# Kernel optimization log

Hardware: AMD Instinct MI355X
Metric: run time of the kernel (lower is better)

## Reference

```python
import jax, jax.numpy as jnp
import numpy as np

N = 50000      # nodes
E = 800000     # edges (avg degree 16)
D = 128        # node_embedding_dim
H = 256        # hidden_dim


def setup_inputs() -> dict:
    key = jax.random.key(0)
    ks = jax.random.split(key, 12)
    init = lambda k, shape, fan: (jax.random.normal(k, shape, jnp.float32) / np.sqrt(fan).astype(np.float32))
    return {
        "node_ids": jnp.arange(N, dtype=jnp.int32),
        "edge_index": jax.random.randint(ks[0], (2, E), 0, N, jnp.int32),
        "neighbour_edge_index": jax.random.randint(ks[1], (2, E), 0, N, jnp.int32),
        "edge_attr": jax.random.uniform(ks[2], (E,), jnp.float32),
        "emb": init(ks[3], (N, D), D),          # Embedding table
        "W_in": init(ks[4], (D, H), D), "b_in": jnp.zeros((H,), jnp.float32),
        "W_out": init(ks[5], (H, D), H), "b_out": jnp.zeros((D,), jnp.float32),
        "W1": init(ks[6], (2 * D, D), 2 * D), "b1": jnp.zeros((D,), jnp.float32),
        "W2": init(ks[7], (D, D), D), "b2": jnp.zeros((D,), jnp.float32),
        "W3": init(ks[8], (D, 1), D), "b3": jnp.zeros((1,), jnp.float32),
    }


def gcn_conv(x, W, b, edge_index, w):
    """PyG GCNConv, add_self_loops=False, normalize=True.
    out_i = b + sum_{(j->i)} d_i^{-1/2} w_ji d_j^{-1/2} (x_j @ W)
    deg_i = sum of incoming edge weights at target node i.
    """
    row, col = edge_index[0], edge_index[1]
    deg = jax.ops.segment_sum(w, col, num_segments=N)
    dinv = jnp.where(deg > 0, 1.0 / jnp.sqrt(deg), 0.0)
    norm = dinv[row] * w * dinv[col]                    # [E]
    h = x @ W                                           # [N, out]
    msg = h[row] * norm[:, None]                        # [E, out]
    return jax.ops.segment_sum(msg, col, num_segments=N) + b


def reference(node_ids, edge_index, neighbour_edge_index, edge_attr,
              emb, W_in, b_in, W_out, b_out, W1, b1, W2, b2, W3, b3):
    x = emb[node_ids]                                   # embedding lookup [N, D]
    x = jax.nn.elu(gcn_conv(x, W_in, b_in, edge_index, edge_attr))
    ones = jnp.ones((neighbour_edge_index.shape[1],), x.dtype)
    x = jax.nn.elu(gcn_conv(x, W_out, b_out, neighbour_edge_index, ones))
    # edge-level gather-concat-MLP decoder
    src, dst = edge_index[0], edge_index[1]
    h = jnp.concatenate([x[src], x[dst]], axis=1)       # [E, 2D]
    h = jax.nn.relu(h @ W1 + b1)
    h = jax.nn.relu(h @ W2 + b2)
    return (h @ W3 + b3).squeeze(-1)                    # [E]
```

## Files before the change

kernel.cpp:

```cpp
#include <hip/hip_runtime.h>
#include <math.h>

#define NN 50000
#define NE 800000

typedef __attribute__((ext_vector_type(8))) short s8_t;
typedef __attribute__((ext_vector_type(4))) float f4_t;

__device__ __forceinline__ short bf16_rne(float v) {
  unsigned u = __float_as_uint(v);
  unsigned r = (u + 0x7FFFu + ((u >> 16) & 1u)) >> 16;
  return (short)r;
}
__device__ __forceinline__ float bf16_tof(short h) {
  return __uint_as_float(((unsigned)(unsigned short)h) << 16);
}
__device__ __forceinline__ void split2(float v, short& hi, short& lo) {
  hi = bf16_rne(v);
  lo = bf16_rne(v - bf16_tof(hi));
}


__global__ __launch_bounds__(256) void k_wcvt(const float* __restrict__ W1,
                                              const float* __restrict__ W2,
                                              const float* __restrict__ W_in,
                                              const float* __restrict__ W_out,
                                              short* __restrict__ w1th,
                                              short* __restrict__ w1tl,
                                              short* __restrict__ w2th,
                                              short* __restrict__ w2tl,
                                              short* __restrict__ winth,
                                              short* __restrict__ wintl,
                                              short* __restrict__ woutth,
                                              short* __restrict__ wouttl) {
  int i = blockIdx.x * 256 + threadIdx.x;
  if (i < 32768) {
    int k = i >> 7, n = i & 127;
    short h, l; split2(W1[i], h, l);
    w1th[n * 256 + k] = h; w1tl[n * 256 + k] = l;
  } else if (i < 49152) {
    int j = i - 32768;
    int k = j >> 7, n = j & 127;
    short h, l; split2(W2[j], h, l);
    w2th[n * 128 + k] = h; w2tl[n * 128 + k] = l;
  } else if (i < 81920) {
    int j = i - 49152;
    int k = j >> 8, n = j & 255;
    short h, l; split2(W_in[j], h, l);
    winth[n * 128 + k] = h; wintl[n * 128 + k] = l;
  } else if (i < 114688) {
    int j = i - 81920;
    int k = j >> 7, n = j & 127;
    short h, l; split2(W_out[j], h, l);
    woutth[n * 256 + k] = h; wouttl[n * 256 + k] = l;
  }
}


__global__ __launch_bounds__(256) void k_hist(const int* __restrict__ ei,
                                              const int* __restrict__ nei,
                                              const float* __restrict__ w,
                                              int* __restrict__ cnt1,
                                              float* __restrict__ deg1,
                                              int* __restrict__ cnt2) {
  int e = blockIdx.x * 256 + threadIdx.x;
  if (e < NE) {
    int c1 = ei[NE + e];
    atomicAdd(&cnt1[c1], 1);
    atomicAdd(&deg1[c1], w[e]);
    atomicAdd(&cnt2[nei[NE + e]], 1);
  }
}

__global__ __launch_bounds__(256) void k_dinvs(const float* __restrict__ deg1,
                                               const int* __restrict__ cnt2,
                                               float* __restrict__ dinv1,
                                               float* __restrict__ dinv2) {
  int i = blockIdx.x * 256 + threadIdx.x;
  if (i < NN) {
    float d1 = deg1[i];
    dinv1[i] = d1 > 0.f ? (1.0f / sqrtf(d1)) : 0.f;
    int c2 = cnt2[i];
    dinv2[i] = c2 > 0 ? (1.0f / sqrtf((float)c2)) : 0.f;
  }
}


#define NCHUNK 196

__global__ __launch_bounds__(256) void k_scan_part(const int* __restrict__ cnt1,
                                                   const int* __restrict__ cnt2,
                                                   int* __restrict__ part) {
  int g = blockIdx.x >= NCHUNK;
  int chunk = g ? blockIdx.x - NCHUNK : blockIdx.x;
  const int* cnt = g ? cnt2 : cnt1;
  int i = chunk * 256 + threadIdx.x;
  int v = (i < NN) ? cnt[i] : 0;
  __shared__ int sd[4];
#pragma unroll
  for (int o = 32; o; o >>= 1) v += __shfl_down(v, o);
  if ((threadIdx.x & 63) == 0) sd[threadIdx.x >> 6] = v;
  __syncthreads();
  if (threadIdx.x == 0) part[blockIdx.x] = sd[0] + sd[1] + sd[2] + sd[3];
}

__global__ __launch_bounds__(256) void k_scan_mid(int* __restrict__ part,
                                                  int* __restrict__ off1_last,
                                                  int* __restrict__ off2_last) {
  __shared__ int sd[256];
  for (int g = 0; g < 2; g++) {
    int base = g * NCHUNK;
    int v = (threadIdx.x < NCHUNK) ? part[base + threadIdx.x] : 0;
    sd[threadIdx.x] = v;
    __syncthreads();
    for (int o = 1; o < 256; o <<= 1) {
      int x = (threadIdx.x >= o) ? sd[threadIdx.x - o] : 0;
      __syncthreads();
      sd[threadIdx.x] += x;
      __syncthreads();
    }
    if (threadIdx.x < NCHUNK) part[base + threadIdx.x] = sd[threadIdx.x] - v;
    if (threadIdx.x == 255) *(g ? off2_last : off1_last) = sd[255];
    __syncthreads();
  }
}

__global__ __launch_bounds__(256) void k_scan_final(const int* __restrict__ cnt1,
                                                    const int* __restrict__ cnt2,
                                                    const int* __restrict__ part,
                                                    int* __restrict__ off1,
                                                    int* __restrict__ pos1,
                                                    int* __restrict__ off2,
                                                    int* __restrict__ pos2) {
  int g = blockIdx.x >= NCHUNK;
  int chunk = g ? blockIdx.x - NCHUNK : blockIdx.x;
  const int* cnt = g ? cnt2 : cnt1;
  int* off = g ? off2 : off1;
  int* pos = g ? pos2 : pos1;
  __shared__ int sd[256];
  int i = chunk * 256 + threadIdx.x;
  int v = (i < NN) ? cnt[i] : 0;
  sd[threadIdx.x] = v;
  __syncthreads();
  for (int o = 1; o < 256; o <<= 1) {
    int x = (threadIdx.x >= o) ? sd[threadIdx.x - o] : 0;
    __syncthreads();
    sd[threadIdx.x] += x;
    __syncthreads();
  }
  if (i < NN) {
    int ex = part[blockIdx.x] + sd[threadIdx.x] - v;
    off[i] = ex; pos[i] = ex;
  }
}


__global__ __launch_bounds__(256) void k_fill(const int* __restrict__ ei,
                                              const int* __restrict__ nei,
                                              const float* __restrict__ w,
                                              const float* __restrict__ dinv1,
                                              const float* __restrict__ dinv2,
                                              int* __restrict__ pos1,
                                              int4* __restrict__ c1pack,
                                              int* __restrict__ pos2,
                                              int2* __restrict__ c2pack) {
  int e = blockIdx.x * 256 + threadIdx.x;
  if (e < NE) {
    int r = ei[e], c = ei[NE + e];
    float nv = dinv1[r] * w[e] * dinv1[c];
    int s = atomicAdd(&pos1[c], 1);
    c1pack[s] = make_int4(r, c, e, __float_as_int(nv));
    int r2 = nei[e], c2v = nei[NE + e];
    float nv2 = dinv2[r2] * dinv2[c2v];
    int s2 = atomicAdd(&pos2[c2v], 1);
    c2pack[s2] = make_int2(r2, __float_as_int(nv2));
  }
}


__global__ __launch_bounds__(256) void k_agg1(const int* __restrict__ off,
                                              const int4* __restrict__ c1pack,
                                              const int* __restrict__ ids,
                                              const float* __restrict__ emb,
                                              short* __restrict__ aggXh,
                                              short* __restrict__ aggXl) {
  int wave = threadIdx.x >> 6, lane = threadIdx.x & 63;
  int h = lane >> 5, sub = lane & 31;
  int node = blockIdx.x * 4 + wave;
  int start = off[node], end = off[node + 1];
  float4 acc = make_float4(0.f, 0.f, 0.f, 0.f);
  int i = start + h;
  for (; i + 14 < end; i += 16) {
    float4 v[8]; float n[8];
#pragma unroll
    for (int k = 0; k < 8; k++) {
      int4 p = c1pack[i + 2 * k];
      n[k] = __int_as_float(p.w);
      v[k] = *(const float4*)(emb + (size_t)ids[p.x] * 128 + sub * 4);
    }
#pragma unroll
    for (int k = 0; k < 8; k++) {
      acc.x = fmaf(n[k], v[k].x, acc.x);
      acc.y = fmaf(n[k], v[k].y, acc.y);
      acc.z = fmaf(n[k], v[k].z, acc.z);
      acc.w = fmaf(n[k], v[k].w, acc.w);
    }
  }
  for (; i < end; i += 2) {
    int4 p = c1pack[i];
    float n0 = __int_as_float(p.w);
    float4 v0 = *(const float4*)(emb + (size_t)ids[p.x] * 128 + sub * 4);
    acc.x = fmaf(n0, v0.x, acc.x);
    acc.y = fmaf(n0, v0.y, acc.y);
    acc.z = fmaf(n0, v0.z, acc.z);
    acc.w = fmaf(n0, v0.w, acc.w);
  }
  acc.x += __shfl_xor(acc.x, 32);
  acc.y += __shfl_xor(acc.y, 32);
  acc.z += __shfl_xor(acc.z, 32);
  acc.w += __shfl_xor(acc.w, 32);
  if (h == 0) {
    short h0, l0, h1, l1, h2, l2, h3, l3;
    split2(acc.x, h0, l0); split2(acc.y, h1, l1);
    split2(acc.z, h2, l2); split2(acc.w, h3, l3);
    uint2 hp, lp;
    hp.x = (unsigned)(unsigned short)h0 | ((unsigned)(unsigned short)h1 << 16);
    hp.y = (unsigned)(unsigned short)h2 | ((unsigned)(unsigned short)h3 << 16);
    lp.x = (unsigned)(unsigned short)l0 | ((unsigned)(unsigned short)l1 << 16);
    lp.y = (unsigned)(unsigned short)l2 | ((unsigned)(unsigned short)l3 << 16);
    *(uint2*)(aggXh + (size_t)node * 128 + sub * 4) = hp;
    *(uint2*)(aggXl + (size_t)node * 128 + sub * 4) = lp;
  }
}


__global__ __launch_bounds__(256) void k_agg2(const int* __restrict__ off,
                                              const int2* __restrict__ c2pack,
                                              const float* __restrict__ h2,
                                              const float* __restrict__ b,
                                              short* __restrict__ xh,
                                              short* __restrict__ xl) {
  int wave = threadIdx.x >> 6, lane = threadIdx.x & 63;
  int h = lane >> 5, sub = lane & 31;
  int node = blockIdx.x * 4 + wave;
  int start = off[node], end = off[node + 1];
  float4 acc = make_float4(0.f, 0.f, 0.f, 0.f);
  int i = start + h;
  for (; i + 14 < end; i += 16) {
    float4 v[8]; float n[8];
#pragma unroll
    for (int k = 0; k < 8; k++) {
      int2 p = c2pack[i + 2 * k];
      n[k] = __int_as_float(p.y);
      v[k] = *(const float4*)(h2 + (size_t)p.x * 128 + sub * 4);
    }
#pragma unroll
    for (int k = 0; k < 8; k++) {
      acc.x = fmaf(n[k], v[k].x, acc.x);
      acc.y = fmaf(n[k], v[k].y, acc.y);
      acc.z = fmaf(n[k], v[k].z, acc.z);
      acc.w = fmaf(n[k], v[k].w, acc.w);
    }
  }
  for (; i < end; i += 2) {
    int2 p = c2pack[i];
    float n0 = __int_as_float(p.y);
    float4 v0 = *(const float4*)(h2 + (size_t)p.x * 128 + sub * 4);
    acc.x = fmaf(n0, v0.x, acc.x);
    acc.y = fmaf(n0, v0.y, acc.y);
    acc.z = fmaf(n0, v0.z, acc.z);
    acc.w = fmaf(n0, v0.w, acc.w);
  }
  acc.x += __shfl_xor(acc.x, 32);
  acc.y += __shfl_xor(acc.y, 32);
  acc.z += __shfl_xor(acc.z, 32);
  acc.w += __shfl_xor(acc.w, 32);
  if (h == 0) {
    float4 bb = *(const float4*)(b + sub * 4);
    float v0 = acc.x + bb.x, v1 = acc.y + bb.y;
    float v2 = acc.z + bb.z, v3 = acc.w + bb.w;
    v0 = v0 > 0.f ? v0 : expm1f(v0);
    v1 = v1 > 0.f ? v1 : expm1f(v1);
    v2 = v2 > 0.f ? v2 : expm1f(v2);
    v3 = v3 > 0.f ? v3 : expm1f(v3);
    short h0, l0, h1, l1, h2s, l2, h3, l3;
    split2(v0, h0, l0); split2(v1, h1, l1);
    split2(v2, h2s, l2); split2(v3, h3, l3);
    uint2 hp, lp;
    hp.x = (unsigned)(unsigned short)h0 | ((unsigned)(unsigned short)h1 << 16);
    hp.y = (unsigned)(unsigned short)h2s | ((unsigned)(unsigned short)h3 << 16);
    lp.x = (unsigned)(unsigned short)l0 | ((unsigned)(unsigned short)l1 << 16);
    lp.y = (unsigned)(unsigned short)l2 | ((unsigned)(unsigned short)l3 << 16);
    *(uint2*)(xh + (size_t)node * 128 + sub * 4) = hp;
    *(uint2*)(xl + (size_t)node * 128 + sub * 4) = lp;
  }
}


__global__ __launch_bounds__(256) void k_gemm1m(const short* __restrict__ aggXh,
                                                const short* __restrict__ aggXl,
                                                const short* __restrict__ winth,
                                                const short* __restrict__ wintl,
                                                const float* __restrict__ b,
                                                short* __restrict__ x1h,
                                                short* __restrict__ x1l) {
  __shared__ short Xh[32 * 136];
  __shared__ short Xl[32 * 136];
  int t = threadIdx.x;
  int n0 = blockIdx.x * 32;
#pragma unroll
  for (int j = 0; j < 2; j++) {
    int i = t + 256 * j;
    int row = i >> 4, q = i & 15;
    int node = n0 + row; if (node >= NN) node = NN - 1;
    *(uint4*)&Xh[row * 136 + q * 8] = *(const uint4*)(aggXh + (size_t)node * 128 + q * 8);
    *(uint4*)&Xl[row * 136 + q * 8] = *(const uint4*)(aggXl + (size_t)node * 128 + q * 8);
  }
  __syncthreads();

  int w = t >> 6, lane = t & 63;
  int quad = lane >> 4, l16 = lane & 15;
  int nb = w * 64;
  int aoff0 = l16 * 136 + quad * 8;
  int aoff1 = (16 + l16) * 136 + quad * 8;

  f4_t acc[2][4];
#pragma unroll
  for (int mi = 0; mi < 2; mi++)
#pragma unroll
    for (int ni = 0; ni < 4; ni++) acc[mi][ni] = (f4_t){0.f, 0.f, 0.f, 0.f};

#pragma unroll
  for (int kb = 0; kb < 4; kb++) {
    int k0 = kb * 32;
    s8_t ah0 = *(const s8_t*)&Xh[aoff0 + k0];
    s8_t ah1 = *(const s8_t*)&Xh[aoff1 + k0];
    s8_t al0 = *(const s8_t*)&Xl[aoff0 + k0];
    s8_t al1 = *(const s8_t*)&Xl[aoff1 + k0];
#pragma unroll
    for (int ni = 0; ni < 4; ni++) {
      int bo = (nb + ni * 16 + l16) * 128 + quad * 8 + k0;
      s8_t bh = *(const s8_t*)(winth + bo);
      s8_t bl = *(const s8_t*)(wintl + bo);
      acc[0][ni] = __builtin_amdgcn_mfma_f32_16x16x32_bf16(ah0, bh, acc[0][ni], 0, 0, 0);
      acc[0][ni] = __builtin_amdgcn_mfma_f32_16x16x32_bf16(ah0, bl, acc[0][ni], 0, 0, 0);
      acc[0][ni] = __builtin_amdgcn_mfma_f32_16x16x32_bf16(al0, bh, acc[0][ni], 0, 0, 0);
      acc[1][ni] = __builtin_amdgcn_mfma_f32_16x16x32_bf16(ah1, bh, acc[1][ni], 0, 0, 0);
      acc[1][ni] = __builtin_amdgcn_mfma_f32_16x16x32_bf16(ah1, bl, acc[1][ni], 0, 0, 0);
      acc[1][ni] = __builtin_amdgcn_mfma_f32_16x16x32_bf16(al1, bh, acc[1][ni], 0, 0, 0);
    }
  }

#pragma unroll
  for (int mi = 0; mi < 2; mi++)
#pragma unroll
    for (int ni = 0; ni < 4; ni++) {
      int col = nb + ni * 16 + l16;
      float bv = b[col];
#pragma unroll
      for (int r = 0; r < 4; r++) {
        int node = n0 + mi * 16 + quad * 4 + r;
        if (node < NN) {
          float v = acc[mi][ni][r] + bv;
          v = v > 0.f ? v : expm1f(v);
          short hh, ll; split2(v, hh, ll);
          x1h[(size_t)node * 256 + col] = hh;
          x1l[(size_t)node * 256 + col] = ll;
        }
      }
    }
}


__global__ __launch_bounds__(256) void k_gemm2m(const short* __restrict__ x1h,
                                                const short* __restrict__ x1l,
                                                const short* __restrict__ woutth,
                                                const short* __restrict__ wouttl,
                                                float* __restrict__ h2) {
  __shared__ short Xh[32 * 264];
  __shared__ short Xl[32 * 264];
  int t = threadIdx.x;
  int n0 = blockIdx.x * 32;
#pragma unroll
  for (int j = 0; j < 4; j++) {
    int i = t + 256 * j;
    int row = i >> 5, q = i & 31;
    int node = n0 + row; if (node >= NN) node = NN - 1;
    *(uint4*)&Xh[row * 264 + q * 8] = *(const uint4*)(x1h + (size_t)node * 256 + q * 8);
    *(uint4*)&Xl[row * 264 + q * 8] = *(const uint4*)(x1l + (size_t)node * 256 + q * 8);
  }
  __syncthreads();

  int w = t >> 6, lane = t & 63;
  int quad = lane >> 4, l16 = lane & 15;
  int nb = w * 32;
  int aoff0 = l16 * 264 + quad * 8;
  int aoff1 = (16 + l16) * 264 + quad * 8;

  f4_t acc[2][2];
#pragma unroll
  for (int mi = 0; mi < 2; mi++)
#pragma unroll
    for (int ni = 0; ni < 2; ni++) acc[mi][ni] = (f4_t){0.f, 0.f, 0.f, 0.f};

#pragma unroll
  for (int kb = 0; kb < 8; kb++) {
    int k0 = kb * 32;
    s8_t ah0 = *(const s8_t*)&Xh[aoff0 + k0];
    s8_t ah1 = *(const s8_t*)&Xh[aoff1 + k0];
    s8_t al0 = *(const s8_t*)&Xl[aoff0 + k0];
    s8_t al1 = *(const s8_t*)&Xl[aoff1 + k0];
#pragma unroll
    for (int ni = 0; ni < 2; ni++) {
      int bo = (nb + ni * 16 + l16) * 256 + quad * 8 + k0;
      s8_t bh = *(const s8_t*)(woutth + bo);
      s8_t bl = *(const s8_t*)(wouttl + bo);
      acc[0][ni] = __builtin_amdgcn_mfma_f32_16x16x32_bf16(ah0, bh, acc[0][ni], 0, 0, 0);
      acc[0][ni] = __builtin_amdgcn_mfma_f32_16x16x32_bf16(ah0, bl, acc[0][ni], 0, 0, 0);
      acc[0][ni] = __builtin_amdgcn_mfma_f32_16x16x32_bf16(al0, bh, acc[0][ni], 0, 0, 0);
      acc[1][ni] = __builtin_amdgcn_mfma_f32_16x16x32_bf16(ah1, bh, acc[1][ni], 0, 0, 0);
      acc[1][ni] = __builtin_amdgcn_mfma_f32_16x16x32_bf16(ah1, bl, acc[1][ni], 0, 0, 0);
      acc[1][ni] = __builtin_amdgcn_mfma_f32_16x16x32_bf16(al1, bh, acc[1][ni], 0, 0, 0);
    }
  }

#pragma unroll
  for (int mi = 0; mi < 2; mi++)
#pragma unroll
    for (int ni = 0; ni < 2; ni++) {
      int col = nb + ni * 16 + l16;
#pragma unroll
      for (int r = 0; r < 4; r++) {
        int node = n0 + mi * 16 + quad * 4 + r;
        if (node < NN) h2[(size_t)node * 128 + col] = acc[mi][ni][r];
      }
    }
}


__global__ __launch_bounds__(256) void k_pab(const short* __restrict__ x2h,
                                             const short* __restrict__ x2l,
                                             const short* __restrict__ w1th,
                                             const short* __restrict__ w1tl,
                                             const float* __restrict__ b1,
                                             float* __restrict__ Pa,
                                             float* __restrict__ Pb) {
  __shared__ short Xh[32 * 136];
  __shared__ short Xl[32 * 136];
  int t = threadIdx.x;
  int n0 = blockIdx.x * 32;
#pragma unroll
  for (int j = 0; j < 2; j++) {
    int i = t + 256 * j;
    int row = i >> 4, q = i & 15;
    int node = n0 + row; if (node >= NN) node = NN - 1;
    *(uint4*)&Xh[row * 136 + q * 8] = *(const uint4*)(x2h + (size_t)node * 128 + q * 8);
    *(uint4*)&Xl[row * 136 + q * 8] = *(const uint4*)(x2l + (size_t)node * 128 + q * 8);
  }
  __syncthreads();

  int w = t >> 6, lane = t & 63;
  int quad = lane >> 4, l16 = lane & 15;
  int nb = w * 32;
  int aoff0 = l16 * 136 + quad * 8;
  int aoff1 = (16 + l16) * 136 + quad * 8;
  int bo0 = (nb + l16) * 256 + quad * 8;
  int bo1 = (nb + 16 + l16) * 256 + quad * 8;

  f4_t aa[2][2], ab[2][2];
#pragma unroll
  for (int mi = 0; mi < 2; mi++)
#pragma unroll
    for (int ni = 0; ni < 2; ni++) {
      aa[mi][ni] = (f4_t){0.f, 0.f, 0.f, 0.f};
      ab[mi][ni] = (f4_t){0.f, 0.f, 0.f, 0.f};
    }

#pragma unroll
  for (int kb = 0; kb < 4; kb++) {
    int k0 = kb * 32;
    s8_t ah0 = *(const s8_t*)&Xh[aoff0 + k0];
    s8_t ah1 = *(const s8_t*)&Xh[aoff1 + k0];
    s8_t al0 = *(const s8_t*)&Xl[aoff0 + k0];
    s8_t al1 = *(const s8_t*)&Xl[aoff1 + k0];
    {
      s8_t bh0 = *(const s8_t*)(w1th + bo0 + k0);
      s8_t bh1 = *(const s8_t*)(w1th + bo1 + k0);
      s8_t bl0 = *(const s8_t*)(w1tl + bo0 + k0);
      s8_t bl1 = *(const s8_t*)(w1tl + bo1 + k0);
      aa[0][0] = __builtin_amdgcn_mfma_f32_16x16x32_bf16(ah0, bh0, aa[0][0], 0, 0, 0);
      aa[0][0] = __builtin_amdgcn_mfma_f32_16x16x32_bf16(ah0, bl0, aa[0][0], 0, 0, 0);
      aa[0][0] = __builtin_amdgcn_mfma_f32_16x16x32_bf16(al0, bh0, aa[0][0], 0, 0, 0);
      aa[0][1] = __builtin_amdgcn_mfma_f32_16x16x32_bf16(ah0, bh1, aa[0][1], 0, 0, 0);
      aa[0][1] = __builtin_amdgcn_mfma_f32_16x16x32_bf16(ah0, bl1, aa[0][1], 0, 0, 0);
      aa[0][1] = __builtin_amdgcn_mfma_f32_16x16x32_bf16(al0, bh1, aa[0][1], 0, 0, 0);
      aa[1][0] = __builtin_amdgcn_mfma_f32_16x16x32_bf16(ah1, bh0, aa[1][0], 0, 0, 0);
      aa[1][0] = __builtin_amdgcn_mfma_f32_16x16x32_bf16(ah1, bl0, aa[1][0], 0, 0, 0);
      aa[1][0] = __builtin_amdgcn_mfma_f32_16x16x32_bf16(al1, bh0, aa[1][0], 0, 0, 0);
      aa[1][1] = __builtin_amdgcn_mfma_f32_16x16x32_bf16(ah1, bh1, aa[1][1], 0, 0, 0);
      aa[1][1] = __builtin_amdgcn_mfma_f32_16x16x32_bf16(ah1, bl1, aa[1][1], 0, 0, 0);
      aa[1][1] = __builtin_amdgcn_mfma_f32_16x16x32_bf16(al1, bh1, aa[1][1], 0, 0, 0);
    }
    {
      s8_t bh0 = *(const s8_t*)(w1th + bo0 + 128 + k0);
      s8_t bh1 = *(const s8_t*)(w1th + bo1 + 128 + k0);
      s8_t bl0 = *(const s8_t*)(w1tl + bo0 + 128 + k0);
      s8_t bl1 = *(const s8_t*)(w1tl + bo1 + 128 + k0);
      ab[0][0] = __builtin_amdgcn_mfma_f32_16x16x32_bf16(ah0, bh0, ab[0][0], 0, 0, 0);
      ab[0][0] = __builtin_amdgcn_mfma_f32_16x16x32_bf16(ah0, bl0, ab[0][0], 0, 0, 0);
      ab[0][0] = __builtin_amdgcn_mfma_f32_16x16x32_bf16(al0, bh0, ab[0][0], 0, 0, 0);
      ab[0][1] = __builtin_amdgcn_mfma_f32_16x16x32_bf16(ah0, bh1, ab[0][1], 0, 0, 0);
      ab[0][1] = __builtin_amdgcn_mfma_f32_16x16x32_bf16(ah0, bl1, ab[0][1], 0, 0, 0);
      ab[0][1] = __builtin_amdgcn_mfma_f32_16x16x32_bf16(al0, bh1, ab[0][1], 0, 0, 0);
      ab[1][0] = __builtin_amdgcn_mfma_f32_16x16x32_bf16(ah1, bh0, ab[1][0], 0, 0, 0);
      ab[1][0] = __builtin_amdgcn_mfma_f32_16x16x32_bf16(ah1, bl0, ab[1][0], 0, 0, 0);
      ab[1][0] = __builtin_amdgcn_mfma_f32_16x16x32_bf16(al1, bh0, ab[1][0], 0, 0, 0);
      ab[1][1] = __builtin_amdgcn_mfma_f32_16x16x32_bf16(ah1, bh1, ab[1][1], 0, 0, 0);
      ab[1][1] = __builtin_amdgcn_mfma_f32_16x16x32_bf16(ah1, bl1, ab[1][1], 0, 0, 0);
      ab[1][1] = __builtin_amdgcn_mfma_f32_16x16x32_bf16(al1, bh1, ab[1][1], 0, 0, 0);
    }
  }

  float b1v0 = b1[nb + l16], b1v1 = b1[nb + 16 + l16];
#pragma unroll
  for (int mi = 0; mi < 2; mi++)
#pragma unroll
    for (int ni = 0; ni < 2; ni++) {
      int col = nb + ni * 16 + l16;
      float bv = ni ? b1v1 : b1v0;
#pragma unroll
      for (int r = 0; r < 4; r++) {
        int node = n0 + mi * 16 + quad * 4 + r;
        if (node < NN) {
          Pa[(size_t)node * 128 + col] = aa[mi][ni][r];
          Pb[(size_t)node * 128 + col] = ab[mi][ni][r] + bv;
        }
      }
    }
}


#define ST 136

__global__ __launch_bounds__(256, 4) void k_decoder(
    const float* __restrict__ Pa, const float* __restrict__ Pb,
    const int4* __restrict__ c1pack,
    const short* __restrict__ w2th, const short* __restrict__ w2tl,
    const float* __restrict__ b2,
    const float* __restrict__ W3, const float* __restrict__ b3,
    float* __restrict__ out) {
  __shared__ short Th[32 * ST];
  __shared__ short Tl[32 * ST];
  __shared__ float part[4][32];

  int t = threadIdx.x;
  int b = blockIdx.x;
  int id = (b & 7) * 3125 + (b >> 3);
  int s0base = id * 32;

#pragma unroll
  for (int j = 0; j < 2; j++) {
    int i = t + 256 * j;
    int le = i >> 4, q = i & 15;
    int4 p = c1pack[s0base + le];
    const float* pa = Pa + (size_t)p.x * 128 + q * 8;
    const float* pb = Pb + (size_t)p.y * 128 + q * 8;
    float4 a0 = *(const float4*)(pa);
    float4 a1 = *(const float4*)(pa + 4);
    float4 c0 = *(const float4*)(pb);
    float4 c1 = *(const float4*)(pb + 4);
    float v[8];
    v[0] = a0.x + c0.x; v[1] = a0.y + c0.y;
    v[2] = a0.z + c0.z; v[3] = a0.w + c0.w;
    v[4] = a1.x + c1.x; v[5] = a1.y + c1.y;
    v[6] = a1.z + c1.z; v[7] = a1.w + c1.w;
    s8_t hv, lv;
#pragma unroll
    for (int k = 0; k < 8; k++) {
      float x = fmaxf(v[k], 0.f);
      short h, l; split2(x, h, l);
      hv[k] = h; lv[k] = l;
    }
    *(s8_t*)&Th[le * ST + q * 8] = hv;
    *(s8_t*)&Tl[le * ST + q * 8] = lv;
  }
  __syncthreads();

  int w = t >> 6, lane = t & 63;
  int quad = lane >> 4, l16 = lane & 15;
  int nb = w * 32;
  float b2v0 = b2[nb + l16], b2v1 = b2[nb + 16 + l16];
  float w3a = W3[nb + l16], w3b = W3[nb + 16 + l16];

  int toff0 = l16 * ST + quad * 8;
  int toff1 = (16 + l16) * ST + quad * 8;
  int coff0 = (nb + l16) * 128 + quad * 8;
  int coff1 = (nb + 16 + l16) * 128 + quad * 8;

  f4_t acc2[2][2];
#pragma unroll
  for (int mi = 0; mi < 2; mi++)
#pragma unroll
    for (int ni = 0; ni < 2; ni++) acc2[mi][ni] = (f4_t){0.f, 0.f, 0.f, 0.f};

#pragma unroll
  for (int kb = 0; kb < 4; kb++) {
    int k0 = kb * 32;
    s8_t ah0 = *(const s8_t*)&Th[toff0 + k0];
    s8_t ah1 = *(const s8_t*)&Th[toff1 + k0];
    s8_t al0 = *(const s8_t*)&Tl[toff0 + k0];
    s8_t al1 = *(const s8_t*)&Tl[toff1 + k0];
    s8_t bh0 = *(const s8_t*)(w2th + coff0 + k0);
    s8_t bh1 = *(const s8_t*)(w2th + coff1 + k0);
    s8_t bl0 = *(const s8_t*)(w2tl + coff0 + k0);
    s8_t bl1 = *(const s8_t*)(w2tl + coff1 + k0);
    acc2[0][0] = __builtin_amdgcn_mfma_f32_16x16x32_bf16(ah0, bh0, acc2[0][0], 0, 0, 0);
    acc2[0][0] = __builtin_amdgcn_mfma_f32_16x16x32_bf16(ah0, bl0, acc2[0][0], 0, 0, 0);
    acc2[0][0] = __builtin_amdgcn_mfma_f32_16x16x32_bf16(al0, bh0, acc2[0][0], 0, 0, 0);
    acc2[0][1] = __builtin_amdgcn_mfma_f32_16x16x32_bf16(ah0, bh1, acc2[0][1], 0, 0, 0);
    acc2[0][1] = __builtin_amdgcn_mfma_f32_16x16x32_bf16(ah0, bl1, acc2[0][1], 0, 0, 0);
    acc2[0][1] = __builtin_amdgcn_mfma_f32_16x16x32_bf16(al0, bh1, acc2[0][1], 0, 0, 0);
    acc2[1][0] = __builtin_amdgcn_mfma_f32_16x16x32_bf16(ah1, bh0, acc2[1][0], 0, 0, 0);
    acc2[1][0] = __builtin_amdgcn_mfma_f32_16x16x32_bf16(ah1, bl0, acc2[1][0], 0, 0, 0);
    acc2[1][0] = __builtin_amdgcn_mfma_f32_16x16x32_bf16(al1, bh0, acc2[1][0], 0, 0, 0);
    acc2[1][1] = __builtin_amdgcn_mfma_f32_16x16x32_bf16(ah1, bh1, acc2[1][1], 0, 0, 0);
    acc2[1][1] = __builtin_amdgcn_mfma_f32_16x16x32_bf16(ah1, bl1, acc2[1][1], 0, 0, 0);
    acc2[1][1] = __builtin_amdgcn_mfma_f32_16x16x32_bf16(al1, bh1, acc2[1][1], 0, 0, 0);
  }

#pragma unroll
  for (int mi = 0; mi < 2; mi++) {
#pragma unroll
    for (int r = 0; r < 4; r++) {
      float pv = fmaxf(acc2[mi][0][r] + b2v0, 0.f) * w3a +
                 fmaxf(acc2[mi][1][r] + b2v1, 0.f) * w3b;
      pv += __shfl_xor(pv, 1);
      pv += __shfl_xor(pv, 2);
      pv += __shfl_xor(pv, 4);
      pv += __shfl_xor(pv, 8);
      if (l16 == 0) part[w][mi * 16 + quad * 4 + r] = pv;
    }
  }
  __syncthreads();

  if (t < 32) {
    float s = part[0][t] + part[1][t] + part[2][t] + part[3][t] + b3[0];
    int4 p = c1pack[s0base + t];
    out[p.z] = s;
  }
}


extern "C" void kernel_launch(void* const* d_in, const int* in_sizes, int n_in,
                              void* d_out, int out_size, void* d_ws, size_t ws_size,
                              hipStream_t stream) {
  const int*   node_ids = (const int*)d_in[0];
  const int*   ei       = (const int*)d_in[1];
  const int*   nei      = (const int*)d_in[2];
  const float* eattr    = (const float*)d_in[3];
  const float* emb      = (const float*)d_in[4];
  const float* W_in     = (const float*)d_in[5];
  const float* b_in     = (const float*)d_in[6];
  const float* W_out    = (const float*)d_in[7];
  const float* b_out    = (const float*)d_in[8];
  const float* W1       = (const float*)d_in[9];
  const float* b1       = (const float*)d_in[10];
  const float* W2       = (const float*)d_in[11];
  const float* b2       = (const float*)d_in[12];
  const float* W3       = (const float*)d_in[13];
  const float* b3       = (const float*)d_in[14];
  float* out = (float*)d_out;

  float* ws    = (float*)d_ws;
  float* bufA  = ws;
  float* bufB  = bufA + (size_t)NN * 128;
  int*   cnt1  = (int*)(bufB + (size_t)NN * 256);
  int*   cnt2  = cnt1 + NN;
  float* deg1  = (float*)(cnt2 + NN);
  float* dinv1 = deg1 + NN;
  float* dinv2 = dinv1 + NN;
  int*   off1  = (int*)(dinv2 + NN);
  int*   pos1  = off1 + NN + 1;
  int*   off2  = pos1 + NN;
  int*   pos2  = off2 + NN + 1;
  int4*  c1pack = (int4*)((((uintptr_t)(pos2 + NN)) + 15) & ~(uintptr_t)15);
  int2*  c2pack = (int2*)(c1pack + NE);
  short* w1th   = (short*)(c2pack + NE);
  short* w1tl   = w1th + 32768;
  short* w2th   = w1tl + 32768;
  short* w2tl   = w2th + 16384;
  short* winth  = w2tl + 16384;
  short* wintl  = winth + 32768;
  short* woutth = wintl + 32768;
  short* wouttl = woutth + 32768;
  int*   part   = (int*)(wouttl + 32768);

  short* aggXh = (short*)bufA;
  short* aggXl = aggXh + (size_t)NN * 128;
  float* h2    = bufA;
  float* Pa    = bufA;
  short* x1h   = (short*)bufB;
  short* x1l   = x1h + (size_t)NN * 256;
  short* x2h   = (short*)bufB;
  short* x2l   = x2h + (size_t)NN * 128;
  float* Pb    = bufB + (size_t)NN * 128;

  k_wcvt<<<448, 256, 0, stream>>>(W1, W2, W_in, W_out,
                                  w1th, w1tl, w2th, w2tl,
                                  winth, wintl, woutth, wouttl);

  hipMemsetAsync(cnt1, 0, 3 * (size_t)NN * sizeof(int), stream);
  k_hist<<<NE / 256, 256, 0, stream>>>(ei, nei, eattr, cnt1, deg1, cnt2);
  k_dinvs<<<(NN + 255) / 256, 256, 0, stream>>>(deg1, cnt2, dinv1, dinv2);
  k_scan_part<<<2 * NCHUNK, 256, 0, stream>>>(cnt1, cnt2, part);
  k_scan_mid<<<1, 256, 0, stream>>>(part, off1 + NN, off2 + NN);
  k_scan_final<<<2 * NCHUNK, 256, 0, stream>>>(cnt1, cnt2, part,
                                               off1, pos1, off2, pos2);
  k_fill<<<NE / 256, 256, 0, stream>>>(ei, nei, eattr, dinv1, dinv2,
                                       pos1, c1pack, pos2, c2pack);

  k_agg1<<<NN / 4, 256, 0, stream>>>(off1, c1pack, node_ids, emb, aggXh, aggXl);
  k_gemm1m<<<(NN + 31) / 32, 256, 0, stream>>>(aggXh, aggXl, winth, wintl,
                                               b_in, x1h, x1l);

  k_gemm2m<<<(NN + 31) / 32, 256, 0, stream>>>(x1h, x1l, woutth, wouttl, h2);
  k_agg2<<<NN / 4, 256, 0, stream>>>(off2, c2pack, h2, b_out, x2h, x2l);

  k_pab<<<(NN + 31) / 32, 256, 0, stream>>>(x2h, x2l, w1th, w1tl, b1, Pa, Pb);

  k_decoder<<<NE / 32, 256, 0, stream>>>(Pa, Pb, c1pack,
                                         w2th, w2tl, b2, W3, b3, out);
}
```

Measured before the change: 760.7 us.

## Fuse the two GCN GEMMs through shared memory and fold dinv into scan

Merges the input-projection and output-projection GEMMs into one kernel. The ELU'd hidden activations are kept in LDS as split bf16 hi/lo instead of being written to and reread from global memory, which removes an N×256 intermediate round trip and one launch. The degree-inverse computation moves into the scan partial kernel to drop another launch. The decoder gather now issues both edge rows' loads up front to raise memory-level parallelism. The cost is more LDS per block for the fused GEMM, which may lower occupancy, and a reshuffled buffer layout for h2, Pb and x2.

```diff
diff --git a/kernel.cpp b/kernel.cpp
--- a/kernel.cpp
+++ b/kernel.cpp
@@ -72,34 +72,33 @@
   }
 }
 
-__global__ __launch_bounds__(256) void k_dinvs(const float* __restrict__ deg1,
-                                               const int* __restrict__ cnt2,
-                                               float* __restrict__ dinv1,
-                                               float* __restrict__ dinv2) {
-  int i = blockIdx.x * 256 + threadIdx.x;
-  if (i < NN) {
-    float d1 = deg1[i];
-    dinv1[i] = d1 > 0.f ? (1.0f / sqrtf(d1)) : 0.f;
-    int c2 = cnt2[i];
-    dinv2[i] = c2 > 0 ? (1.0f / sqrtf((float)c2)) : 0.f;
-  }
-}
-
 
 #define NCHUNK 196
 
 __global__ __launch_bounds__(256) void k_scan_part(const int* __restrict__ cnt1,
                                                    const int* __restrict__ cnt2,
+                                                   const float* __restrict__ deg1,
+                                                   float* __restrict__ dinv1,
+                                                   float* __restrict__ dinv2,
                                                    int* __restrict__ part) {
   int g = blockIdx.x >= NCHUNK;
   int chunk = g ? blockIdx.x - NCHUNK : blockIdx.x;
   const int* cnt = g ? cnt2 : cnt1;
   int i = chunk * 256 + threadIdx.x;
   int v = (i < NN) ? cnt[i] : 0;
+  if (i < NN) {
+    if (!g) {
+      float d1 = deg1[i];
+      dinv1[i] = d1 > 0.f ? (1.0f / sqrtf(d1)) : 0.f;
+    } else {
+      dinv2[i] = v > 0 ? (1.0f / sqrtf((float)v)) : 0.f;
+    }
+  }
   __shared__ int sd[4];
-#pragma unroll
-  for (int o = 32; o; o >>= 1) v += __shfl_down(v, o);
-  if ((threadIdx.x & 63) == 0) sd[threadIdx.x >> 6] = v;
+  int r = v;
+#pragma unroll
+  for (int o = 32; o; o >>= 1) r += __shfl_down(r, o);
+  if ((threadIdx.x & 63) == 0) sd[threadIdx.x >> 6] = r;
   __syncthreads();
   if (threadIdx.x == 0) part[blockIdx.x] = sd[0] + sd[1] + sd[2] + sd[3];
 }
@@ -297,15 +296,18 @@
 }
 
 
-__global__ __launch_bounds__(256) void k_gemm1m(const short* __restrict__ aggXh,
+__global__ __launch_bounds__(256) void k_gemm12(const short* __restrict__ aggXh,
                                                 const short* __restrict__ aggXl,
                                                 const short* __restrict__ winth,
                                                 const short* __restrict__ wintl,
                                                 const float* __restrict__ b,
-                                                short* __restrict__ x1h,
-                                                short* __restrict__ x1l) {
+                                                const short* __restrict__ woutth,
+                                                const short* __restrict__ wouttl,
+                                                float* __restrict__ h2) {
   __shared__ short Xh[32 * 136];
   __shared__ short Xl[32 * 136];
+  __shared__ short Yh[32 * 264];
+  __shared__ short Yl[32 * 264];
   int t = threadIdx.x;
   int n0 = blockIdx.x * 32;
 #pragma unroll
@@ -320,121 +322,102 @@
 
   int w = t >> 6, lane = t & 63;
   int quad = lane >> 4, l16 = lane & 15;
-  int nb = w * 64;
-  int aoff0 = l16 * 136 + quad * 8;
-  int aoff1 = (16 + l16) * 136 + quad * 8;
-
-  f4_t acc[2][4];
-#pragma unroll
-  for (int mi = 0; mi < 2; mi++)
-#pragma unroll
-    for (int ni = 0; ni < 4; ni++) acc[mi][ni] = (f4_t){0.f, 0.f, 0.f, 0.f};
-
-#pragma unroll
-  for (int kb = 0; kb < 4; kb++) {
-    int k0 = kb * 32;
-    s8_t ah0 = *(const s8_t*)&Xh[aoff0 + k0];
-    s8_t ah1 = *(const s8_t*)&Xh[aoff1 + k0];
-    s8_t al0 = *(const s8_t*)&Xl[aoff0 + k0];
-    s8_t al1 = *(const s8_t*)&Xl[aoff1 + k0];
-#pragma unroll
-    for (int ni = 0; ni < 4; ni++) {
-      int bo = (nb + ni * 16 + l16) * 128 + quad * 8 + k0;
-      s8_t bh = *(const s8_t*)(winth + bo);
-      s8_t bl = *(const s8_t*)(wintl + bo);
-      acc[0][ni] = __builtin_amdgcn_mfma_f32_16x16x32_bf16(ah0, bh, acc[0][ni], 0, 0, 0);
-      acc[0][ni] = __builtin_amdgcn_mfma_f32_16x16x32_bf16(ah0, bl, acc[0][ni], 0, 0, 0);
-      acc[0][ni] = __builtin_amdgcn_mfma_f32_16x16x32_bf16(al0, bh, acc[0][ni], 0, 0, 0);
-      acc[1][ni] = __builtin_amdgcn_mfma_f32_16x16x32_bf16(ah1, bh, acc[1][ni], 0, 0, 0);
-      acc[1][ni] = __builtin_amdgcn_mfma_f32_16x16x32_bf16(ah1, bl, acc[1][ni], 0, 0, 0);
-      acc[1][ni] = __builtin_amdgcn_mfma_f32_16x16x32_bf16(al1, bh, acc[1][ni], 0, 0, 0);
-    }
-  }
-
-#pragma unroll
-  for (int mi = 0; mi < 2; mi++)
-#pragma unroll
-    for (int ni = 0; ni < 4; ni++) {
-      int col = nb + ni * 16 + l16;
-      float bv = b[col];
-#pragma unroll
-      for (int r = 0; r < 4; r++) {
-        int node = n0 + mi * 16 + quad * 4 + r;
-        if (node < NN) {
+
+  {
+    int nb = w * 64;
+    int aoff0 = l16 * 136 + quad * 8;
+    int aoff1 = (16 + l16) * 136 + quad * 8;
+
+    f4_t acc[2][4];
+#pragma unroll
+    for (int mi = 0; mi < 2; mi++)
+#pragma unroll
+      for (int ni = 0; ni < 4; ni++) acc[mi][ni] = (f4_t){0.f, 0.f, 0.f, 0.f};
+
+#pragma unroll
+    for (int kb = 0; kb < 4; kb++) {
+      int k0 = kb * 32;
+      s8_t ah0 = *(const s8_t*)&Xh[aoff0 + k0];
+      s8_t ah1 = *(const s8_t*)&Xh[aoff1 + k0];
+      s8_t al0 = *(const s8_t*)&Xl[aoff0 + k0];
+      s8_t al1 = *(const s8_t*)&Xl[aoff1 + k0];
+#pragma unroll
+      for (int ni = 0; ni < 4; ni++) {
+        int bo = (nb + ni * 16 + l16) * 128 + quad * 8 + k0;
+        s8_t bh = *(const s8_t*)(winth + bo);
+        s8_t bl = *(const s8_t*)(wintl + bo);
+        acc[0][ni] = __builtin_amdgcn_mfma_f32_16x16x32_bf16(ah0, bh, acc[0][ni], 0, 0, 0);
+        acc[0][ni] = __builtin_amdgcn_mfma_f32_16x16x32_bf16(ah0, bl, acc[0][ni], 0, 0, 0);
+        acc[0][ni] = __builtin_amdgcn_mfma_f32_16x16x32_bf16(al0, bh, acc[0][ni], 0, 0, 0);
+        acc[1][ni] = __builtin_amdgcn_mfma_f32_16x16x32_bf16(ah1, bh, acc[1][ni], 0, 0, 0);
+        acc[1][ni] = __builtin_amdgcn_mfma_f32_16x16x32_bf16(ah1, bl, acc[1][ni], 0, 0, 0);
+        acc[1][ni] = __builtin_amdgcn_mfma_f32_16x16x32_bf16(al1, bh, acc[1][ni], 0, 0, 0);
+      }
+    }
+
+#pragma unroll
+    for (int mi = 0; mi < 2; mi++)
+#pragma unroll
+      for (int ni = 0; ni < 4; ni++) {
+        int col = nb + ni * 16 + l16;
+        float bv = b[col];
+#pragma unroll
+        for (int r = 0; r < 4; r++) {
+          int row = mi * 16 + quad * 4 + r;
           float v = acc[mi][ni][r] + bv;
           v = v > 0.f ? v : expm1f(v);
           short hh, ll; split2(v, hh, ll);
-          x1h[(size_t)node * 256 + col] = hh;
-          x1l[(size_t)node * 256 + col] = ll;
+          Yh[row * 264 + col] = hh;
+          Yl[row * 264 + col] = ll;
         }
       }
-    }
-}
-
-
-__global__ __launch_bounds__(256) void k_gemm2m(const short* __restrict__ x1h,
-                                                const short* __restrict__ x1l,
-                                                const short* __restrict__ woutth,
-                                                const short* __restrict__ wouttl,
-                                                float* __restrict__ h2) {
-  __shared__ short Xh[32 * 264];
-  __shared__ short Xl[32 * 264];
-  int t = threadIdx.x;
-  int n0 = blockIdx.x * 32;
-#pragma unroll
-  for (int j = 0; j < 4; j++) {
-    int i = t + 256 * j;
-    int row = i >> 5, q = i & 31;
-    int node = n0 + row; if (node >= NN) node = NN - 1;
-    *(uint4*)&Xh[row * 264 + q * 8] = *(const uint4*)(x1h + (size_t)node * 256 + q * 8);
-    *(uint4*)&Xl[row * 264 + q * 8] = *(const uint4*)(x1l + (size_t)node * 256 + q * 8);
   }
   __syncthreads();
 
-  int w = t >> 6, lane = t & 63;
-  int quad = lane >> 4, l16 = lane & 15;
-  int nb = w * 32;
-  int aoff0 = l16 * 264 + quad * 8;
-  int aoff1 = (16 + l16) * 264 + quad * 8;
-
-  f4_t acc[2][2];
-#pragma unroll
-  for (int mi = 0; mi < 2; mi++)
-#pragma unroll
-    for (int ni = 0; ni < 2; ni++) acc[mi][ni] = (f4_t){0.f, 0.f, 0.f, 0.f};
-
-#pragma unroll
-  for (int kb = 0; kb < 8; kb++) {
-    int k0 = kb * 32;
-    s8_t ah0 = *(const s8_t*)&Xh[aoff0 + k0];
-    s8_t ah1 = *(const s8_t*)&Xh[aoff1 + k0];
-    s8_t al0 = *(const s8_t*)&Xl[aoff0 + k0];
-    s8_t al1 = *(const s8_t*)&Xl[aoff1 + k0];
-#pragma unroll
-    for (int ni = 0; ni < 2; ni++) {
-      int bo = (nb + ni * 16 + l16) * 256 + quad * 8 + k0;
-      s8_t bh = *(const s8_t*)(woutth + bo);
-      s8_t bl = *(const s8_t*)(wouttl + bo);
-      acc[0][ni] = __builtin_amdgcn_mfma_f32_16x16x32_bf16(ah0, bh, acc[0][ni], 0, 0, 0);
-      acc[0][ni] = __builtin_amdgcn_mfma_f32_16x16x32_bf16(ah0, bl, acc[0][ni], 0, 0, 0);
-      acc[0][ni] = __builtin_amdgcn_mfma_f32_16x16x32_bf16(al0, bh, acc[0][ni], 0, 0, 0);
-      acc[1][ni] = __builtin_amdgcn_mfma_f32_16x16x32_bf16(ah1, bh, acc[1][ni], 0, 0, 0);
-      acc[1][ni] = __builtin_amdgcn_mfma_f32_16x16x32_bf16(ah1, bl, acc[1][ni], 0, 0, 0);
-      acc[1][ni] = __builtin_amdgcn_mfma_f32_16x16x32_bf16(al1, bh, acc[1][ni], 0, 0, 0);
-    }
-  }
-
-#pragma unroll
-  for (int mi = 0; mi < 2; mi++)
-#pragma unroll
-    for (int ni = 0; ni < 2; ni++) {
-      int col = nb + ni * 16 + l16;
-#pragma unroll
-      for (int r = 0; r < 4; r++) {
-        int node = n0 + mi * 16 + quad * 4 + r;
-        if (node < NN) h2[(size_t)node * 128 + col] = acc[mi][ni][r];
+  {
+    int nb = w * 32;
+    int aoff0 = l16 * 264 + quad * 8;
+    int aoff1 = (16 + l16) * 264 + quad * 8;
+
+    f4_t acc[2][2];
+#pragma unroll
+    for (int mi = 0; mi < 2; mi++)
+#pragma unroll
+      for (int ni = 0; ni < 2; ni++) acc[mi][ni] = (f4_t){0.f, 0.f, 0.f, 0.f};
+
+#pragma unroll
+    for (int kb = 0; kb < 8; kb++) {
+      int k0 = kb * 32;
+      s8_t ah0 = *(const s8_t*)&Yh[aoff0 + k0];
+      s8_t ah1 = *(const s8_t*)&Yh[aoff1 + k0];
+      s8_t al0 = *(const s8_t*)&Yl[aoff0 + k0];
+      s8_t al1 = *(const s8_t*)&Yl[aoff1 + k0];
+#pragma unroll
+      for (int ni = 0; ni < 2; ni++) {
+        int bo = (nb + ni * 16 + l16) * 256 + quad * 8 + k0;
+        s8_t bh = *(const s8_t*)(woutth + bo);
+        s8_t bl = *(const s8_t*)(wouttl + bo);
+        acc[0][ni] = __builtin_amdgcn_mfma_f32_16x16x32_bf16(ah0, bh, acc[0][ni], 0, 0, 0);
+        acc[0][ni] = __builtin_amdgcn_mfma_f32_16x16x32_bf16(ah0, bl, acc[0][ni], 0, 0, 0);
+        acc[0][ni] = __builtin_amdgcn_mfma_f32_16x16x32_bf16(al0, bh, acc[0][ni], 0, 0, 0);
+        acc[1][ni] = __builtin_amdgcn_mfma_f32_16x16x32_bf16(ah1, bh, acc[1][ni], 0, 0, 0);
+        acc[1][ni] = __builtin_amdgcn_mfma_f32_16x16x32_bf16(ah1, bl, acc[1][ni], 0, 0, 0);
+        acc[1][ni] = __builtin_amdgcn_mfma_f32_16x16x32_bf16(al1, bh, acc[1][ni], 0, 0, 0);
       }
     }
+
+#pragma unroll
+    for (int mi = 0; mi < 2; mi++)
+#pragma unroll
+      for (int ni = 0; ni < 2; ni++) {
+        int col = nb + ni * 16 + l16;
+#pragma unroll
+        for (int r = 0; r < 4; r++) {
+          int node = n0 + mi * 16 + quad * 4 + r;
+          if (node < NN) h2[(size_t)node * 128 + col] = acc[mi][ni][r];
+        }
+      }
+  }
 }
 
 
@@ -558,31 +541,46 @@
   int id = (b & 7) * 3125 + (b >> 3);
   int s0base = id * 32;
 
-#pragma unroll
-  for (int j = 0; j < 2; j++) {
-    int i = t + 256 * j;
-    int le = i >> 4, q = i & 15;
-    int4 p = c1pack[s0base + le];
-    const float* pa = Pa + (size_t)p.x * 128 + q * 8;
-    const float* pb = Pb + (size_t)p.y * 128 + q * 8;
-    float4 a0 = *(const float4*)(pa);
-    float4 a1 = *(const float4*)(pa + 4);
-    float4 c0 = *(const float4*)(pb);
-    float4 c1 = *(const float4*)(pb + 4);
-    float v[8];
-    v[0] = a0.x + c0.x; v[1] = a0.y + c0.y;
-    v[2] = a0.z + c0.z; v[3] = a0.w + c0.w;
-    v[4] = a1.x + c1.x; v[5] = a1.y + c1.y;
-    v[6] = a1.z + c1.z; v[7] = a1.w + c1.w;
-    s8_t hv, lv;
+  {
+    int le0 = t >> 4, q = t & 15;
+    int4 p0 = c1pack[s0base + le0];
+    int4 p1 = c1pack[s0base + le0 + 16];
+    const float* pa0 = Pa + (size_t)p0.x * 128 + q * 8;
+    const float* pb0 = Pb + (size_t)p0.y * 128 + q * 8;
+    const float* pa1 = Pa + (size_t)p1.x * 128 + q * 8;
+    const float* pb1 = Pb + (size_t)p1.y * 128 + q * 8;
+    float4 ra0 = *(const float4*)(pa0);
+    float4 ra1 = *(const float4*)(pa0 + 4);
+    float4 rb0 = *(const float4*)(pb0);
+    float4 rb1 = *(const float4*)(pb0 + 4);
+    float4 ra2 = *(const float4*)(pa1);
+    float4 ra3 = *(const float4*)(pa1 + 4);
+    float4 rb2 = *(const float4*)(pb1);
+    float4 rb3 = *(const float4*)(pb1 + 4);
+
+    float v0[8], v1[8];
+    v0[0] = ra0.x + rb0.x; v0[1] = ra0.y + rb0.y;
+    v0[2] = ra0.z + rb0.z; v0[3] = ra0.w + rb0.w;
+    v0[4] = ra1.x + rb1.x; v0[5] = ra1.y + rb1.y;
+    v0[6] = ra1.z + rb1.z; v0[7] = ra1.w + rb1.w;
+    v1[0] = ra2.x + rb2.x; v1[1] = ra2.y + rb2.y;
+    v1[2] = ra2.z + rb2.z; v1[3] = ra2.w + rb2.w;
+    v1[4] = ra3.x + rb3.x; v1[5] = ra3.y + rb3.y;
+    v1[6] = ra3.z + rb3.z; v1[7] = ra3.w + rb3.w;
+
+    s8_t hv0, lv0, hv1, lv1;
 #pragma unroll
     for (int k = 0; k < 8; k++) {
-      float x = fmaxf(v[k], 0.f);
-      short h, l; split2(x, h, l);
-      hv[k] = h; lv[k] = l;
-    }
-    *(s8_t*)&Th[le * ST + q * 8] = hv;
-    *(s8_t*)&Tl[le * ST + q * 8] = lv;
+      float x0 = fmaxf(v0[k], 0.f);
+      float x1 = fmaxf(v1[k], 0.f);
+      short hh, ll;
+      split2(x0, hh, ll); hv0[k] = hh; lv0[k] = ll;
+      split2(x1, hh, ll); hv1[k] = hh; lv1[k] = ll;
+    }
+    *(s8_t*)&Th[le0 * ST + q * 8] = hv0;
+    *(s8_t*)&Tl[le0 * ST + q * 8] = lv0;
+    *(s8_t*)&Th[(le0 + 16) * ST + q * 8] = hv1;
+    *(s8_t*)&Tl[(le0 + 16) * ST + q * 8] = lv1;
   }
   __syncthreads();
 
@@ -697,13 +695,11 @@
 
   short* aggXh = (short*)bufA;
   short* aggXl = aggXh + (size_t)NN * 128;
-  float* h2    = bufA;
   float* Pa    = bufA;
-  short* x1h   = (short*)bufB;
-  short* x1l   = x1h + (size_t)NN * 256;
-  short* x2h   = (short*)bufB;
+  float* h2    = bufB;
+  float* Pb    = bufB;
+  short* x2h   = (short*)(bufB + (size_t)NN * 128);
   short* x2l   = x2h + (size_t)NN * 128;
-  float* Pb    = bufB + (size_t)NN * 128;
 
   k_wcvt<<<448, 256, 0, stream>>>(W1, W2, W_in, W_out,
                                   w1th, w1tl, w2th, w2tl,
@@ -711,8 +707,7 @@
 
   hipMemsetAsync(cnt1, 0, 3 * (size_t)NN * sizeof(int), stream);
   k_hist<<<NE / 256, 256, 0, stream>>>(ei, nei, eattr, cnt1, deg1, cnt2);
-  k_dinvs<<<(NN + 255) / 256, 256, 0, stream>>>(deg1, cnt2, dinv1, dinv2);
-  k_scan_part<<<2 * NCHUNK, 256, 0, stream>>>(cnt1, cnt2, part);
+  k_scan_part<<<2 * NCHUNK, 256, 0, stream>>>(cnt1, cnt2, deg1, dinv1, dinv2, part);
   k_scan_mid<<<1, 256, 0, stream>>>(part, off1 + NN, off2 + NN);
   k_scan_final<<<2 * NCHUNK, 256, 0, stream>>>(cnt1, cnt2, part,
                                                off1, pos1, off2, pos2);
@@ -720,10 +715,9 @@
                                        pos1, c1pack, pos2, c2pack);
 
   k_agg1<<<NN / 4, 256, 0, stream>>>(off1, c1pack, node_ids, emb, aggXh, aggXl);
-  k_gemm1m<<<(NN + 31) / 32, 256, 0, stream>>>(aggXh, aggXl, winth, wintl,
-                                               b_in, x1h, x1l);
-
-  k_gemm2m<<<(NN + 31) / 32, 256, 0, stream>>>(x1h, x1l, woutth, wouttl, h2);
+  k_gemm12<<<(NN + 31) / 32, 256, 0, stream>>>(aggXh, aggXl, winth, wintl, b_in,
+                                               woutth, wouttl, h2);
+
   k_agg2<<<NN / 4, 256, 0, stream>>>(off2, c2pack, h2, b_out, x2h, x2l);
 
   k_pab<<<(NN + 31) / 32, 256, 0, stream>>>(x2h, x2l, w1th, w1tl, b1, Pa, Pb);
```

Measured after the change: 730.2 us. 1.04x faster.
